# Performance work log

Measured on AMD Instinct MI355X. Metric: run time of the kernel, lower is better.

The kernel has to match this reference:

```python
import jax, jax.numpy as jnp
import numpy as np
import math

B, S, D, H = 2, 2048, 1024, 16
DK = D // H
THETA = 10000.0

def _rope_tables(seq_len, dk, theta):
    freqs = 1.0 / theta ** (np.arange(0, dk, 2)[: dk // 2].astype(np.float32) / dk)
    t = np.arange(seq_len, dtype=np.float32)
    ang = np.outer(t, freqs)  # [S, dk/2]
    return jnp.asarray(np.cos(ang)), jnp.asarray(np.sin(ang))

def setup_inputs() -> dict:
    key = jax.random.key(0)
    ks = jax.random.split(key, 12)
    init = lambda k, shape: (0.02 * jax.random.normal(k, shape)).astype(jnp.float32)
    cos, sin = _rope_tables(S, DK, THETA)
    mask = jnp.tril(jnp.ones((S, S), dtype=jnp.int32))[None, None]  # [1,1,S,S] causal
    return {
        'Q': jax.random.normal(ks[0], (B, S, D), jnp.float32),
        'K': jax.random.normal(ks[1], (B, S, D), jnp.float32),
        'V': jax.random.normal(ks[2], (B, S, D), jnp.float32),
        'mask': mask,
        'Wq_w': init(ks[3], (D, D)), 'Wq_b': init(ks[4], (D,)),
        'Wk_w': init(ks[5], (D, D)), 'Wk_b': init(ks[6], (D,)),
        'Wv_w': init(ks[7], (D, D)), 'Wv_b': init(ks[8], (D,)),
        'Wo_w': init(ks[9], (D, D)), 'Wo_b': init(ks[10], (D,)),
        'cos': cos, 'sin': sin,
    }

def _apply_rope(x, cos, sin):
    # x: [B, S, H, DK]; cos/sin: [S, DK/2]
    x1 = x[..., 0::2]
    x2 = x[..., 1::2]
    c = cos[None, :, None, :]
    s = sin[None, :, None, :]
    out_even = x1 * c - x2 * s
    out_odd = x1 * s + x2 * c
    return jnp.stack([out_even, out_odd], axis=-1).reshape(x.shape)

def reference(Q, K, V, mask, Wq_w, Wq_b, Wk_w, Wk_b, Wv_w, Wv_b, Wo_w, Wo_b, cos, sin):
    b, s, d = Q.shape
    q = (Q @ Wq_w.T + Wq_b).reshape(b, s, H, DK)
    k = (K @ Wk_w.T + Wk_b).reshape(b, s, H, DK)
    v = (V @ Wv_w.T + Wv_b).reshape(b, s, H, DK)
    q = _apply_rope(q, cos[:s], sin[:s])
    k = _apply_rope(k, cos[:s], sin[:s])
    # [B,H,S,DK]
    q = q.transpose(0, 2, 1, 3)
    k = k.transpose(0, 2, 1, 3)
    v = v.transpose(0, 2, 1, 3)
    scores = jnp.einsum('bhqd,bhkd->bhqk', q, k) / math.sqrt(DK)
    scores = jnp.where(mask == 0, jnp.float32(-1e9), scores)
    probs = jax.nn.softmax(scores, axis=-1)
    out = jnp.einsum('bhqk,bhkd->bhqd', probs, v)  # [B,H,S,DK]
    out = out.transpose(0, 2, 1, 3).reshape(b, s, d)
    return out @ Wo_w.T + Wo_b
```

## Files before the change

### kernel.cpp

```cpp
#include <hip/hip_runtime.h>
#include <cstdint>
#include <cstddef>


typedef __bf16 bf16x8 __attribute__((ext_vector_type(8)));
typedef float floatx4 __attribute__((ext_vector_type(4)));

#define DI __device__ __forceinline__

DI unsigned short f2bf(float f) {
  union { float f; unsigned int u; } v; v.f = f;
  unsigned int r = v.u + 0x7fffu + ((v.u >> 16) & 1u);
  return (unsigned short)(r >> 16);
}

DI unsigned short bfb(float f) {
  __bf16 h = (__bf16)f;
  union { __bf16 h; unsigned short u; } c; c.h = h;
  return c.u;
}

__global__ void cvt_all(const float* __restrict__ Q, const float* __restrict__ K,
                        const float* __restrict__ V, const float* __restrict__ Wq,
                        const float* __restrict__ Wk, const float* __restrict__ Wv,
                        const float* __restrict__ Wo, unsigned short* __restrict__ dst) {
  int i = blockIdx.x * blockDim.x + threadIdx.x;
  const float* s;
  int off;
  if (i < 3145728) {
    if (i < 1048576) { s = Q; off = i; }
    else if (i < 2097152) { s = K; off = i - 1048576; }
    else { s = V; off = i - 2097152; }
  } else {
    int j = i - 3145728;
    int wsel = j >> 18;
    off = j & 262143;
    s = (wsel == 0) ? Wq : (wsel == 1) ? Wk : (wsel == 2) ? Wv : Wo;
  }
  float4 f = reinterpret_cast<const float4*>(s)[off];
  ushort4 o;
  o.x = f2bf(f.x); o.y = f2bf(f.y); o.z = f2bf(f.z); o.w = f2bf(f.w);
  reinterpret_cast<ushort4*>(dst)[i] = o;
}

__global__ __launch_bounds__(256)
void gemm_qkv(const unsigned short* __restrict__ Qb, const unsigned short* __restrict__ Kb,
              const unsigned short* __restrict__ Vb, const unsigned short* __restrict__ Wq,
              const unsigned short* __restrict__ Wk, const unsigned short* __restrict__ Wv,
              const float* __restrict__ bq, const float* __restrict__ bk,
              const float* __restrict__ bv, unsigned short* __restrict__ qh,
              unsigned short* __restrict__ kh, unsigned short* __restrict__ vtp,
              const float* __restrict__ cosT, const float* __restrict__ sinT) {
  __shared__ unsigned short As[2][128 * 32];
  __shared__ unsigned short Bs[2][128 * 32];

  const int id = blockIdx.x;
  const int xb = id / 96;
  const int rem = id - xb * 96;
  const int proj = rem >> 5;
  const int yb = rem & 31;

  const unsigned short* X = (proj == 0) ? Qb : (proj == 1) ? Kb : Vb;
  const unsigned short* W = (proj == 0) ? Wq : (proj == 1) ? Wk : Wv;
  const float* bias = (proj == 0) ? bq : (proj == 1) ? bk : bv;
  unsigned short* outB = (proj == 0) ? qh : (proj == 1) ? kh : vtp;

  const int t = threadIdx.x;
  const int lane = t & 63;
  const int w = t >> 6;
  const int row0 = yb * 128;
  const int col0 = xb * 128;
  const int wm = (w >> 1) * 64;
  const int wn = (w & 1) * 64;
  const int fr = lane & 15;
  const int fk = (lane >> 4) * 8;
  const int rbase = (lane >> 4) * 4;

  const int c0 = t, c1 = t + 256;
  const unsigned short* gA0 = X + (size_t)(row0 + (c0 >> 2)) * 1024 + (c0 & 3) * 8;
  const unsigned short* gA1 = X + (size_t)(row0 + (c1 >> 2)) * 1024 + (c1 & 3) * 8;
  const unsigned short* gB0 = W + (size_t)(col0 + (c0 >> 2)) * 1024 + (c0 & 3) * 8;
  const unsigned short* gB1 = W + (size_t)(col0 + (c1 >> 2)) * 1024 + (c1 & 3) * 8;

  floatx4 acc[4][4];
#pragma unroll
  for (int i = 0; i < 4; ++i)
#pragma unroll
    for (int j = 0; j < 4; ++j)
      acc[i][j] = (floatx4){0.f, 0.f, 0.f, 0.f};

  uint4 ra0, ra1, rb0, rb1;
  auto gload = [&](int k0) {
    ra0 = *reinterpret_cast<const uint4*>(gA0 + k0);
    ra1 = *reinterpret_cast<const uint4*>(gA1 + k0);
    rb0 = *reinterpret_cast<const uint4*>(gB0 + k0);
    rb1 = *reinterpret_cast<const uint4*>(gB1 + k0);
  };
  auto swrite = [&](int buf) {
    *reinterpret_cast<uint4*>(&As[buf][c0 * 8]) = ra0;
    *reinterpret_cast<uint4*>(&As[buf][c1 * 8]) = ra1;
    *reinterpret_cast<uint4*>(&Bs[buf][c0 * 8]) = rb0;
    *reinterpret_cast<uint4*>(&Bs[buf][c1 * 8]) = rb1;
  };

  gload(0);
  swrite(0);
  __syncthreads();

  for (int kb = 0; kb < 32; ++kb) {
    const int cur = kb & 1;
    if (kb + 1 < 32) gload((kb + 1) * 32);

    bf16x8 af[4], bfr[4];
#pragma unroll
    for (int i = 0; i < 4; ++i)
      af[i] = *reinterpret_cast<const bf16x8*>(&As[cur][(wm + i * 16 + fr) * 32 + fk]);
#pragma unroll
    for (int j = 0; j < 4; ++j)
      bfr[j] = *reinterpret_cast<const bf16x8*>(&Bs[cur][(wn + j * 16 + fr) * 32 + fk]);
    if (proj == 2) {
#pragma unroll
      for (int i = 0; i < 4; ++i)
#pragma unroll
        for (int j = 0; j < 4; ++j)
          acc[i][j] = __builtin_amdgcn_mfma_f32_16x16x32_bf16(bfr[j], af[i], acc[i][j], 0, 0, 0);
    } else {
#pragma unroll
      for (int i = 0; i < 4; ++i)
#pragma unroll
        for (int j = 0; j < 4; ++j)
          acc[i][j] = __builtin_amdgcn_mfma_f32_16x16x32_bf16(af[i], bfr[j], acc[i][j], 0, 0, 0);
    }

    if (kb + 1 < 32) swrite(cur ^ 1);
    __syncthreads();
  }

  if (proj < 2) {
#pragma unroll
    for (int j = 0; j < 4; ++j) {
      const int col = col0 + wn + j * 16 + fr;
      const float bvv = bias[col];
#pragma unroll
      for (int i = 0; i < 4; ++i) {
#pragma unroll
        for (int r = 0; r < 4; ++r) {
          const int row = row0 + wm + i * 16 + rbase + r;
          float v = acc[i][j][r] + bvv;
          const int bb = row >> 11, sp = row & 2047, hh = col >> 6, dk = col & 63;
          float p = __shfl_xor(v, 1);
          const int i2 = (col & 63) >> 1;
          const float cv = cosT[sp * 32 + i2];
          const float sv = sinT[sp * 32 + i2];
          float res = ((col & 1) == 0) ? (v * cv - p * sv) : (p * sv + v * cv);
          if (proj == 0) res *= 0.125f;
          outB[(((size_t)(bb * 16 + hh)) * 2048 + sp) * 64 + dk] = f2bf(res);
        }
      }
    }
  } else {
#pragma unroll
    for (int j = 0; j < 4; ++j) {
#pragma unroll
      for (int r = 0; r < 4; ++r) {
        const int dkc = col0 + wn + j * 16 + rbase + r;
        const float bvv = bias[dkc];
        const int hh = dkc >> 6, dk = dkc & 63;
#pragma unroll
        for (int i = 0; i < 4; ++i) {
          const int spf = row0 + wm + i * 16 + fr;
          const int bb = spf >> 11, sp = spf & 2047;
          vtp[(((size_t)(bb * 16 + hh)) * 64 + dk) * 2048 + sp] = f2bf(acc[i][j][r] + bvv);
        }
      }
    }
  }
}

__global__ __launch_bounds__(256)
void gemm_out(const unsigned short* __restrict__ X, const unsigned short* __restrict__ W,
              const float* __restrict__ bias, float* __restrict__ outF) {
  __shared__ unsigned short As[2][64 * 32];
  __shared__ unsigned short Bs[2][128 * 32];

  const int id = blockIdx.x;
  const int xb = id >> 6;
  const int yb = id & 63;

  const int t = threadIdx.x;
  const int lane = t & 63;
  const int w = t >> 6;
  const int row0 = yb * 64;
  const int col0 = xb * 128;
  const int wm = (w >> 1) * 32;
  const int wn = (w & 1) * 64;
  const int fr = lane & 15;
  const int fk = (lane >> 4) * 8;
  const int rbase = (lane >> 4) * 4;

  const int c0 = t, c1 = t + 256;
  const unsigned short* gA0 = X + (size_t)(row0 + (c0 >> 2)) * 1024 + (c0 & 3) * 8;
  const unsigned short* gB0 = W + (size_t)(col0 + (c0 >> 2)) * 1024 + (c0 & 3) * 8;
  const unsigned short* gB1 = W + (size_t)(col0 + (c1 >> 2)) * 1024 + (c1 & 3) * 8;

  floatx4 acc[2][4];
#pragma unroll
  for (int i = 0; i < 2; ++i)
#pragma unroll
    for (int j = 0; j < 4; ++j)
      acc[i][j] = (floatx4){0.f, 0.f, 0.f, 0.f};

  uint4 ra0, rb0, rb1;
  auto gload = [&](int k0) {
    ra0 = *reinterpret_cast<const uint4*>(gA0 + k0);
    rb0 = *reinterpret_cast<const uint4*>(gB0 + k0);
    rb1 = *reinterpret_cast<const uint4*>(gB1 + k0);
  };
  auto swrite = [&](int buf) {
    *reinterpret_cast<uint4*>(&As[buf][c0 * 8]) = ra0;
    *reinterpret_cast<uint4*>(&Bs[buf][c0 * 8]) = rb0;
    *reinterpret_cast<uint4*>(&Bs[buf][c1 * 8]) = rb1;
  };

  gload(0);
  swrite(0);
  __syncthreads();

  for (int kb = 0; kb < 32; ++kb) {
    const int cur = kb & 1;
    if (kb + 1 < 32) gload((kb + 1) * 32);

    bf16x8 af[2], bfr[4];
#pragma unroll
    for (int i = 0; i < 2; ++i)
      af[i] = *reinterpret_cast<const bf16x8*>(&As[cur][(wm + i * 16 + fr) * 32 + fk]);
#pragma unroll
    for (int j = 0; j < 4; ++j)
      bfr[j] = *reinterpret_cast<const bf16x8*>(&Bs[cur][(wn + j * 16 + fr) * 32 + fk]);
#pragma unroll
    for (int i = 0; i < 2; ++i)
#pragma unroll
      for (int j = 0; j < 4; ++j)
        acc[i][j] = __builtin_amdgcn_mfma_f32_16x16x32_bf16(af[i], bfr[j], acc[i][j], 0, 0, 0);

    if (kb + 1 < 32) swrite(cur ^ 1);
    __syncthreads();
  }

#pragma unroll
  for (int j = 0; j < 4; ++j) {
    const int col = col0 + wn + j * 16 + fr;
    const float bvv = bias[col];
#pragma unroll
    for (int i = 0; i < 2; ++i)
#pragma unroll
      for (int r = 0; r < 4; ++r) {
        const int row = row0 + wm + i * 16 + rbase + r;
        outF[(size_t)row * 1024 + col] = acc[i][j][r] + bvv;
      }
  }
}

__global__ __launch_bounds__(256)
void flash_attn(const unsigned short* __restrict__ qh,
                const unsigned short* __restrict__ kh,
                const unsigned short* __restrict__ vt,
                unsigned short* __restrict__ out) {
  __shared__ unsigned short Ks[2][64 * 64];
  __shared__ unsigned short Ps[8][16 * 64];

  const int t = threadIdx.x, lane = t & 63, w = t >> 6;
  const int g = lane >> 4;
  const int fr = lane & 15;
  const int fk = g * 8;
  const int rbase = g * 4;
  const int id = blockIdx.x;
  const int qbA = id >> 5;
  const int bh = id & 31;
  const int qbB = 31 - qbA;
  const int qwA = qbA * 64 + w * 16;
  const int qwB = qbB * 64 + w * 16;

  const size_t baseQK = (size_t)bh * 2048 * 64;
  const size_t baseV = (size_t)bh * 64 * 2048;

  bf16x8 qfA[2], qfB[2];
  qfA[0] = *reinterpret_cast<const bf16x8*>(&qh[baseQK + (size_t)(qwA + fr) * 64 + fk]);
  qfA[1] = *reinterpret_cast<const bf16x8*>(&qh[baseQK + (size_t)(qwA + fr) * 64 + 32 + fk]);
  qfB[0] = *reinterpret_cast<const bf16x8*>(&qh[baseQK + (size_t)(qwB + fr) * 64 + fk]);
  qfB[1] = *reinterpret_cast<const bf16x8*>(&qh[baseQK + (size_t)(qwB + fr) * 64 + 32 + fk]);

  const unsigned short* vP = vt + baseV + (size_t)fr * 2048;

  floatx4 oA[4], oB[4];
  float lA[4], lB[4];
#pragma unroll
  for (int i = 0; i < 4; ++i) {
    oA[i] = (floatx4){0.f, 0.f, 0.f, 0.f};
    oB[i] = (floatx4){0.f, 0.f, 0.f, 0.f};
    lA[i] = 0.f; lB[i] = 0.f;
  }

  const int sc0 = t, sc1 = t + 256;
  const int r0 = sc0 >> 3, cc0 = sc0 & 7, d0 = (r0 * 8 + (cc0 ^ (r0 & 7))) * 8;
  const int r1 = sc1 >> 3, cc1 = sc1 & 7, d1 = (r1 * 8 + (cc1 ^ (r1 & 7))) * 8;

  uint4 rk0, rk1;
  auto gload = [&](int kb) {
    const int k0 = kb * 64;
    rk0 = *reinterpret_cast<const uint4*>(kh + baseQK + (size_t)(k0 + r0) * 64 + cc0 * 8);
    rk1 = *reinterpret_cast<const uint4*>(kh + baseQK + (size_t)(k0 + r1) * 64 + cc1 * 8);
  };
  auto swrite = [&](int buf) {
    *reinterpret_cast<uint4*>(&Ks[buf][d0]) = rk0;
    *reinterpret_cast<uint4*>(&Ks[buf][d1]) = rk1;
  };

  const int nkb = qbB + 1;
  gload(0);
  swrite(0);
  __syncthreads();

  for (int kb = 0; kb < nkb; ++kb) {
    const int cur = kb & 1;
    if (kb + 1 < nkb) gload(kb + 1);
    const int k0 = kb * 64;
    const bool aAct = (kb <= qbA);

    bf16x8 vf[4][2];
#pragma unroll
    for (int id2 = 0; id2 < 4; ++id2)
#pragma unroll
      for (int kk = 0; kk < 2; ++kk)
        vf[id2][kk] = *reinterpret_cast<const bf16x8*>(
            &vP[(size_t)(id2 * 16) * 2048 + k0 + kk * 32 + fk]);

    bf16x8 kf[4][2];
#pragma unroll
    for (int j = 0; j < 4; ++j)
#pragma unroll
      for (int kk = 0; kk < 2; ++kk)
        kf[j][kk] = *reinterpret_cast<const bf16x8*>(
            &Ks[cur][(j * 16 + fr) * 64 + ((((kk << 2) | g) ^ (fr & 7)) << 3)]);

    floatx4 sB[4], sA[4];
#pragma unroll
    for (int j = 0; j < 4; ++j) {
      sB[j] = (floatx4){0.f, 0.f, 0.f, 0.f};
      sA[j] = (floatx4){0.f, 0.f, 0.f, 0.f};
    }
#pragma unroll
    for (int j = 0; j < 4; ++j)
#pragma unroll
      for (int kk = 0; kk < 2; ++kk)
        sB[j] = __builtin_amdgcn_mfma_f32_16x16x32_bf16(qfB[kk], kf[j][kk], sB[j], 0, 0, 0);
    if (aAct) {
#pragma unroll
      for (int j = 0; j < 4; ++j)
#pragma unroll
        for (int kk = 0; kk < 2; ++kk)
          sA[j] = __builtin_amdgcn_mfma_f32_16x16x32_bf16(qfA[kk], kf[j][kk], sA[j], 0, 0, 0);
    }

    if (k0 + 63 > qwB) {
#pragma unroll
      for (int j = 0; j < 4; ++j)
#pragma unroll
        for (int r = 0; r < 4; ++r)
          if (k0 + j * 16 + fr > qwB + rbase + r) sB[j][r] = -1e30f;
    }
    if (aAct && k0 + 63 > qwA) {
#pragma unroll
      for (int j = 0; j < 4; ++j)
#pragma unroll
        for (int r = 0; r < 4; ++r)
          if (k0 + j * 16 + fr > qwA + rbase + r) sA[j][r] = -1e30f;
    }

#pragma unroll
    for (int j = 0; j < 4; ++j) {
      const int chb = (j * 16 + fr) >> 3;
      const int cin = fr & 7;
#pragma unroll
      for (int r = 0; r < 4; ++r) {
        const int row = rbase + r;
        float pB = __expf(sB[j][r]);
        lB[r] += pB;
        Ps[w][row * 64 + ((chb ^ (row & 7)) << 3) + cin] = bfb(pB);
      }
    }
    if (aAct) {
#pragma unroll
      for (int j = 0; j < 4; ++j) {
        const int chb = (j * 16 + fr) >> 3;
        const int cin = fr & 7;
#pragma unroll
        for (int r = 0; r < 4; ++r) {
          const int row = rbase + r;
          float pA = __expf(sA[j][r]);
          lA[r] += pA;
          Ps[w + 4][row * 64 + ((chb ^ (row & 7)) << 3) + cin] = bfb(pA);
        }
      }
    }

    bf16x8 pB2[2], pA2[2];
#pragma unroll
    for (int kk = 0; kk < 2; ++kk)
      pB2[kk] = *reinterpret_cast<const bf16x8*>(
          &Ps[w][fr * 64 + ((((kk << 2) | g) ^ (fr & 7)) << 3)]);
#pragma unroll
    for (int kk = 0; kk < 2; ++kk)
#pragma unroll
      for (int id2 = 0; id2 < 4; ++id2)
        oB[id2] = __builtin_amdgcn_mfma_f32_16x16x32_bf16(pB2[kk], vf[id2][kk], oB[id2], 0, 0, 0);
    if (aAct) {
#pragma unroll
      for (int kk = 0; kk < 2; ++kk)
        pA2[kk] = *reinterpret_cast<const bf16x8*>(
            &Ps[w + 4][fr * 64 + ((((kk << 2) | g) ^ (fr & 7)) << 3)]);
#pragma unroll
      for (int kk = 0; kk < 2; ++kk)
#pragma unroll
        for (int id2 = 0; id2 < 4; ++id2)
          oA[id2] = __builtin_amdgcn_mfma_f32_16x16x32_bf16(pA2[kk], vf[id2][kk], oA[id2], 0, 0, 0);
    }

    if (kb + 1 < nkb) swrite(cur ^ 1);
    __syncthreads();
  }

#pragma unroll
  for (int r = 0; r < 4; ++r) {
#pragma unroll
    for (int d = 1; d < 16; d <<= 1) {
      lB[r] += __shfl_xor(lB[r], d);
      lA[r] += __shfl_xor(lA[r], d);
    }
  }

  const int bb = bh >> 4, hh = bh & 15;
#pragma unroll
  for (int id2 = 0; id2 < 4; ++id2)
#pragma unroll
    for (int r = 0; r < 4; ++r) {
      const int qrA = qwA + rbase + r;
      const int qrB = qwB + rbase + r;
      out[((size_t)(bb * 2048 + qrA)) * 1024 + hh * 64 + id2 * 16 + fr] = bfb(oA[id2][r] / lA[r]);
      out[((size_t)(bb * 2048 + qrB)) * 1024 + hh * 64 + id2 * 16 + fr] = bfb(oB[id2][r] / lB[r]);
    }
}

extern "C" void kernel_launch(void* const* d_in, const int* in_sizes, int n_in,
                              void* d_out, int out_size, void* d_ws, size_t ws_size,
                              hipStream_t stream) {
  const float* Q  = (const float*)d_in[0];
  const float* K  = (const float*)d_in[1];
  const float* V  = (const float*)d_in[2];
  const float* Wq = (const float*)d_in[4];
  const float* bq = (const float*)d_in[5];
  const float* Wk = (const float*)d_in[6];
  const float* bk = (const float*)d_in[7];
  const float* Wv = (const float*)d_in[8];
  const float* bv = (const float*)d_in[9];
  const float* Wo = (const float*)d_in[10];
  const float* bo = (const float*)d_in[11];
  const float* cosT = (const float*)d_in[12];
  const float* sinT = (const float*)d_in[13];

  char* ws = (char*)d_ws;
  const size_t MB = 1024 * 1024;
  unsigned short* Qb  = (unsigned short*)(ws + 0 * MB);
  unsigned short* Kb  = (unsigned short*)(ws + 8 * MB);
  unsigned short* Vb  = (unsigned short*)(ws + 16 * MB);
  unsigned short* Wqb = (unsigned short*)(ws + 24 * MB);
  unsigned short* Wkb = (unsigned short*)(ws + 26 * MB);
  unsigned short* Wvb = (unsigned short*)(ws + 28 * MB);
  unsigned short* Wob = (unsigned short*)(ws + 30 * MB);
  unsigned short* qh  = (unsigned short*)(ws + 32 * MB);
  unsigned short* khp = (unsigned short*)(ws + 40 * MB);
  unsigned short* vtp = (unsigned short*)(ws + 48 * MB);
  unsigned short* ao  = (unsigned short*)(ws + 56 * MB);

  cvt_all<<<16384, 256, 0, stream>>>(Q, K, V, Wq, Wk, Wv, Wo, (unsigned short*)ws);

  gemm_qkv<<<768, 256, 0, stream>>>(Qb, Kb, Vb, Wqb, Wkb, Wvb, bq, bk, bv,
                                    qh, khp, vtp, cosT, sinT);
  flash_attn<<<512, 256, 0, stream>>>(qh, khp, vtp, ao);
  gemm_out<<<512, 256, 0, stream>>>(ao, Wob, bo, (float*)d_out);
}
```

Baseline: 263.8 us.

## Stage V through LDS with K, process 128-key blocks, use exp2 softmax

The flash attention kernel now loads V tiles into shared memory alongside K instead of reading V fragments directly from global memory each iteration. Each loop step now covers two 64-key sub-tiles, halving the number of barriers and loads per key. The Q scale absorbs log2(e), so the kernel uses exp2f in place of __expf. This raises LDS usage (four K and four V buffers) and register pressure, which may reduce occupancy.

```diff
diff --git a/kernel.cpp b/kernel.cpp
--- a/kernel.cpp
+++ b/kernel.cpp
@@ -153,7 +153,7 @@
           const float cv = cosT[sp * 32 + i2];
           const float sv = sinT[sp * 32 + i2];
           float res = ((col & 1) == 0) ? (v * cv - p * sv) : (p * sv + v * cv);
-          if (proj == 0) res *= 0.125f;
+          if (proj == 0) res *= 0.18033688f;
           outB[(((size_t)(bb * 16 + hh)) * 2048 + sp) * 64 + dk] = f2bf(res);
         }
       }
@@ -266,7 +266,8 @@
                 const unsigned short* __restrict__ kh,
                 const unsigned short* __restrict__ vt,
                 unsigned short* __restrict__ out) {
-  __shared__ unsigned short Ks[2][64 * 64];
+  __shared__ unsigned short Ks[4][64 * 64];
+  __shared__ unsigned short Vs[4][64 * 64];
   __shared__ unsigned short Ps[8][16 * 64];
 
   const int t = threadIdx.x, lane = t & 63, w = t >> 6;
@@ -290,8 +291,6 @@
   qfB[0] = *reinterpret_cast<const bf16x8*>(&qh[baseQK + (size_t)(qwB + fr) * 64 + fk]);
   qfB[1] = *reinterpret_cast<const bf16x8*>(&qh[baseQK + (size_t)(qwB + fr) * 64 + 32 + fk]);
 
-  const unsigned short* vP = vt + baseV + (size_t)fr * 2048;
-
   floatx4 oA[4], oB[4];
   float lA[4], lB[4];
 #pragma unroll
@@ -305,18 +304,29 @@
   const int r0 = sc0 >> 3, cc0 = sc0 & 7, d0 = (r0 * 8 + (cc0 ^ (r0 & 7))) * 8;
   const int r1 = sc1 >> 3, cc1 = sc1 & 7, d1 = (r1 * 8 + (cc1 ^ (r1 & 7))) * 8;
 
-  uint4 rk0, rk1;
+  uint4 rk[2][2], rv[2][2];
   auto gload = [&](int kb) {
-    const int k0 = kb * 64;
-    rk0 = *reinterpret_cast<const uint4*>(kh + baseQK + (size_t)(k0 + r0) * 64 + cc0 * 8);
-    rk1 = *reinterpret_cast<const uint4*>(kh + baseQK + (size_t)(k0 + r1) * 64 + cc1 * 8);
+    const int k0 = kb * 128;
+#pragma unroll
+    for (int s = 0; s < 2; ++s) {
+      rk[0][s] = *reinterpret_cast<const uint4*>(kh + baseQK + (size_t)(k0 + s * 64 + r0) * 64 + cc0 * 8);
+      rk[1][s] = *reinterpret_cast<const uint4*>(kh + baseQK + (size_t)(k0 + s * 64 + r1) * 64 + cc1 * 8);
+      rv[0][s] = *reinterpret_cast<const uint4*>(vt + baseV + (size_t)r0 * 2048 + k0 + s * 64 + cc0 * 8);
+      rv[1][s] = *reinterpret_cast<const uint4*>(vt + baseV + (size_t)r1 * 2048 + k0 + s * 64 + cc1 * 8);
+    }
   };
   auto swrite = [&](int buf) {
-    *reinterpret_cast<uint4*>(&Ks[buf][d0]) = rk0;
-    *reinterpret_cast<uint4*>(&Ks[buf][d1]) = rk1;
+#pragma unroll
+    for (int s = 0; s < 2; ++s) {
+      *reinterpret_cast<uint4*>(&Ks[2 * buf + s][d0]) = rk[0][s];
+      *reinterpret_cast<uint4*>(&Ks[2 * buf + s][d1]) = rk[1][s];
+      *reinterpret_cast<uint4*>(&Vs[2 * buf + s][d0]) = rv[0][s];
+      *reinterpret_cast<uint4*>(&Vs[2 * buf + s][d1]) = rv[1][s];
+    }
   };
 
-  const int nkb = qbB + 1;
+  const int nkb64 = qbB + 1;
+  const int nkb = (nkb64 + 1) >> 1;
   gload(0);
   swrite(0);
   __syncthreads();
@@ -324,72 +334,58 @@
   for (int kb = 0; kb < nkb; ++kb) {
     const int cur = kb & 1;
     if (kb + 1 < nkb) gload(kb + 1);
-    const int k0 = kb * 64;
-    const bool aAct = (kb <= qbA);
-
-    bf16x8 vf[4][2];
-#pragma unroll
-    for (int id2 = 0; id2 < 4; ++id2)
-#pragma unroll
-      for (int kk = 0; kk < 2; ++kk)
-        vf[id2][kk] = *reinterpret_cast<const bf16x8*>(
-            &vP[(size_t)(id2 * 16) * 2048 + k0 + kk * 32 + fk]);
-
-    bf16x8 kf[4][2];
-#pragma unroll
-    for (int j = 0; j < 4; ++j)
-#pragma unroll
-      for (int kk = 0; kk < 2; ++kk)
-        kf[j][kk] = *reinterpret_cast<const bf16x8*>(
-            &Ks[cur][(j * 16 + fr) * 64 + ((((kk << 2) | g) ^ (fr & 7)) << 3)]);
-
-    floatx4 sB[4], sA[4];
-#pragma unroll
-    for (int j = 0; j < 4; ++j) {
-      sB[j] = (floatx4){0.f, 0.f, 0.f, 0.f};
-      sA[j] = (floatx4){0.f, 0.f, 0.f, 0.f};
-    }
-#pragma unroll
-    for (int j = 0; j < 4; ++j)
-#pragma unroll
-      for (int kk = 0; kk < 2; ++kk)
-        sB[j] = __builtin_amdgcn_mfma_f32_16x16x32_bf16(qfB[kk], kf[j][kk], sB[j], 0, 0, 0);
-    if (aAct) {
+
+#pragma unroll
+    for (int h = 0; h < 2; ++h) {
+      const int t64 = 2 * kb + h;
+      if (t64 > qbB) break;
+      const int k0 = t64 * 64;
+      const bool aAct = (t64 <= qbA);
+      const unsigned short* ks = Ks[2 * cur + h];
+      const unsigned short* vs = Vs[2 * cur + h];
+
+      bf16x8 kf[4][2];
 #pragma unroll
       for (int j = 0; j < 4; ++j)
 #pragma unroll
         for (int kk = 0; kk < 2; ++kk)
-          sA[j] = __builtin_amdgcn_mfma_f32_16x16x32_bf16(qfA[kk], kf[j][kk], sA[j], 0, 0, 0);
-    }
-
-    if (k0 + 63 > qwB) {
+          kf[j][kk] = *reinterpret_cast<const bf16x8*>(
+              &ks[(j * 16 + fr) * 64 + ((((kk << 2) | g) ^ (fr & 7)) << 3)]);
+
+      floatx4 sB[4], sA[4];
+#pragma unroll
+      for (int j = 0; j < 4; ++j) {
+        sB[j] = (floatx4){0.f, 0.f, 0.f, 0.f};
+        sA[j] = (floatx4){0.f, 0.f, 0.f, 0.f};
+      }
 #pragma unroll
       for (int j = 0; j < 4; ++j)
 #pragma unroll
-        for (int r = 0; r < 4; ++r)
-          if (k0 + j * 16 + fr > qwB + rbase + r) sB[j][r] = -1e30f;
-    }
-    if (aAct && k0 + 63 > qwA) {
-#pragma unroll
-      for (int j = 0; j < 4; ++j)
-#pragma unroll
-        for (int r = 0; r < 4; ++r)
-          if (k0 + j * 16 + fr > qwA + rbase + r) sA[j][r] = -1e30f;
-    }
-
-#pragma unroll
-    for (int j = 0; j < 4; ++j) {
-      const int chb = (j * 16 + fr) >> 3;
-      const int cin = fr & 7;
-#pragma unroll
-      for (int r = 0; r < 4; ++r) {
-        const int row = rbase + r;
-        float pB = __expf(sB[j][r]);
-        lB[r] += pB;
-        Ps[w][row * 64 + ((chb ^ (row & 7)) << 3) + cin] = bfb(pB);
-      }
-    }
-    if (aAct) {
+        for (int kk = 0; kk < 2; ++kk)
+          sB[j] = __builtin_amdgcn_mfma_f32_16x16x32_bf16(qfB[kk], kf[j][kk], sB[j], 0, 0, 0);
+      if (aAct) {
+#pragma unroll
+        for (int j = 0; j < 4; ++j)
+#pragma unroll
+          for (int kk = 0; kk < 2; ++kk)
+            sA[j] = __builtin_amdgcn_mfma_f32_16x16x32_bf16(qfA[kk], kf[j][kk], sA[j], 0, 0, 0);
+      }
+
+      if (k0 + 63 > qwB) {
+#pragma unroll
+        for (int j = 0; j < 4; ++j)
+#pragma unroll
+          for (int r = 0; r < 4; ++r)
+            if (k0 + j * 16 + fr > qwB + rbase + r) sB[j][r] = -1e30f;
+      }
+      if (aAct && k0 + 63 > qwA) {
+#pragma unroll
+        for (int j = 0; j < 4; ++j)
+#pragma unroll
+          for (int r = 0; r < 4; ++r)
+            if (k0 + j * 16 + fr > qwA + rbase + r) sA[j][r] = -1e30f;
+      }
+
 #pragma unroll
       for (int j = 0; j < 4; ++j) {
         const int chb = (j * 16 + fr) >> 3;
@@ -397,33 +393,53 @@
 #pragma unroll
         for (int r = 0; r < 4; ++r) {
           const int row = rbase + r;
-          float pA = __expf(sA[j][r]);
-          lA[r] += pA;
-          Ps[w + 4][row * 64 + ((chb ^ (row & 7)) << 3) + cin] = bfb(pA);
+          float pB = exp2f(sB[j][r]);
+          lB[r] += pB;
+          Ps[w][row * 64 + ((chb ^ (row & 7)) << 3) + cin] = bfb(pB);
         }
       }
-    }
-
-    bf16x8 pB2[2], pA2[2];
-#pragma unroll
-    for (int kk = 0; kk < 2; ++kk)
-      pB2[kk] = *reinterpret_cast<const bf16x8*>(
-          &Ps[w][fr * 64 + ((((kk << 2) | g) ^ (fr & 7)) << 3)]);
-#pragma unroll
-    for (int kk = 0; kk < 2; ++kk)
+      if (aAct) {
+#pragma unroll
+        for (int j = 0; j < 4; ++j) {
+          const int chb = (j * 16 + fr) >> 3;
+          const int cin = fr & 7;
+#pragma unroll
+          for (int r = 0; r < 4; ++r) {
+            const int row = rbase + r;
+            float pA = exp2f(sA[j][r]);
+            lA[r] += pA;
+            Ps[w + 4][row * 64 + ((chb ^ (row & 7)) << 3) + cin] = bfb(pA);
+          }
+        }
+      }
+
+      bf16x8 vf[4][2], pB2[2], pA2[2];
 #pragma unroll
       for (int id2 = 0; id2 < 4; ++id2)
-        oB[id2] = __builtin_amdgcn_mfma_f32_16x16x32_bf16(pB2[kk], vf[id2][kk], oB[id2], 0, 0, 0);
-    if (aAct) {
+#pragma unroll
+        for (int kk = 0; kk < 2; ++kk)
+          vf[id2][kk] = *reinterpret_cast<const bf16x8*>(
+              &vs[(id2 * 16 + fr) * 64 + ((((kk << 2) | g) ^ (fr & 7)) << 3)]);
 #pragma unroll
       for (int kk = 0; kk < 2; ++kk)
-        pA2[kk] = *reinterpret_cast<const bf16x8*>(
-            &Ps[w + 4][fr * 64 + ((((kk << 2) | g) ^ (fr & 7)) << 3)]);
+        pB2[kk] = *reinterpret_cast<const bf16x8*>(
+            &Ps[w][fr * 64 + ((((kk << 2) | g) ^ (fr & 7)) << 3)]);
 #pragma unroll
       for (int kk = 0; kk < 2; ++kk)
 #pragma unroll
         for (int id2 = 0; id2 < 4; ++id2)
-          oA[id2] = __builtin_amdgcn_mfma_f32_16x16x32_bf16(pA2[kk], vf[id2][kk], oA[id2], 0, 0, 0);
+          oB[id2] = __builtin_amdgcn_mfma_f32_16x16x32_bf16(pB2[kk], vf[id2][kk], oB[id2], 0, 0, 0);
+      if (aAct) {
+#pragma unroll
+        for (int kk = 0; kk < 2; ++kk)
+          pA2[kk] = *reinterpret_cast<const bf16x8*>(
+              &Ps[w + 4][fr * 64 + ((((kk << 2) | g) ^ (fr & 7)) << 3)]);
+#pragma unroll
+        for (int kk = 0; kk < 2; ++kk)
+#pragma unroll
+          for (int id2 = 0; id2 < 4; ++id2)
+            oA[id2] = __builtin_amdgcn_mfma_f32_16x16x32_bf16(pA2[kk], vf[id2][kk], oA[id2], 0, 0, 0);
+      }
     }
 
     if (kb + 1 < nkb) swrite(cur ^ 1);
```

New measurement: 288.9 us. +9.5%, slower.
